# Kernel optimization log

Measured on AMD Instinct MI355X. Metric: run time of the kernel, lower is better.

Reference implementation:

```python
import jax, jax.numpy as jnp
import numpy as np

B, S, D, H = 2, 4096, 512, 8
HD = D // H  # 64


def setup_inputs() -> dict:
    key = jax.random.key(0)
    ks = jax.random.split(key, 9)
    def lin_init(kw, kb, fan_in, fan_out):
        bound = 1.0 / np.sqrt(fan_in)
        W = jax.random.uniform(kw, (fan_in, fan_out), minval=-bound, maxval=bound, dtype=jnp.float32)
        b = jax.random.uniform(kb, (fan_out,), minval=-bound, maxval=bound, dtype=jnp.float32)
        return W, b
    Wq, bq = lin_init(ks[0], ks[1], D, D)
    Wk, bk = lin_init(ks[2], ks[3], D, D)
    Wv, bv = lin_init(ks[4], ks[5], D, D)
    query = jax.random.normal(ks[6], (B, S, D), dtype=jnp.float32)
    key_in = jax.random.normal(ks[7], (B, S, D), dtype=jnp.float32)
    value = jax.random.normal(ks[8], (B, S, D), dtype=jnp.float32)
    return {"query": query, "key": key_in, "value": value,
            "Wq": Wq, "bq": bq, "Wk": Wk, "bk": bk, "Wv": Wv, "bv": bv}


def _split_heads(x):
    # [B, S, D] -> [B, H, S, HD]
    b, s, _ = x.shape
    return x.reshape(b, s, H, HD).transpose(0, 2, 1, 3)


def reference(query, key, value, Wq, bq, Wk, bk, Wv, bv):
    Q = _split_heads(query @ Wq + bq)
    K = _split_heads(key @ Wk + bk)
    V = _split_heads(value @ Wv + bv)
    scale = 1.0 / np.sqrt(HD).astype(np.float32)
    # scores: [B, H, Sq, Sk]
    scores = jnp.einsum('bhqd,bhkd->bhqk', Q, K) * scale
    weights = jax.nn.softmax(scores, axis=-1)
    att = jnp.einsum('bhqk,bhkd->bhqd', weights, V)
    # [B, H, S, HD] -> [B, S, D]
    return att.transpose(0, 2, 1, 3).reshape(query.shape[0], query.shape[1], D)
```

## Files before the change

kernel.cpp:

```cpp
#include <hip/hip_runtime.h>
#include <hip/hip_bf16.h>
#include <cstdint>


typedef __bf16   bf16x8 __attribute__((ext_vector_type(8)));
typedef _Float16 f16x8  __attribute__((ext_vector_type(8)));
typedef float    f32x4  __attribute__((ext_vector_type(4)));
typedef float    f32x16 __attribute__((ext_vector_type(16)));
typedef unsigned int   u32;
typedef unsigned int   u32x4 __attribute__((ext_vector_type(4)));
typedef unsigned short u16;

#define NB  2
#define SEQ 4096
#define DIM 512
#define NH  8
#define HD  64
#define WSZ (DIM * DIM)
#define QSZ (NB * NH * SEQ * HD)

__device__ __forceinline__ u16 f2bf(float f) {
    __bf16 h = (__bf16)f; return __builtin_bit_cast(u16, h);
}
__device__ __forceinline__ u16 f2h(float f) {
    _Float16 h = (_Float16)f; return __builtin_bit_cast(u16, h);
}
__device__ __forceinline__ u32 pack_pkrtz(float a, float b) {
    auto pk = __builtin_amdgcn_cvt_pkrtz(a, b);
    return __builtin_bit_cast(u32, pk);
}
__device__ __forceinline__ bf16x8 cvt8p(float4 a, float4 b) {
    bf16x8 o;
    o[0]=(__bf16)a.x; o[1]=(__bf16)a.y; o[2]=(__bf16)a.z; o[3]=(__bf16)a.w;
    o[4]=(__bf16)b.x; o[5]=(__bf16)b.y; o[6]=(__bf16)b.z; o[7]=(__bf16)b.w;
    return o;
}
__device__ __forceinline__ void dma16(const u16* g, u16* l) {
    __builtin_amdgcn_global_load_lds(
        (const __attribute__((address_space(1))) u32*)g,
        (__attribute__((address_space(3))) u32*)l, 16, 0, 0);
}

__global__ __launch_bounds__(256) void wt_kernel(
    const float* __restrict__ Wq, const float* __restrict__ Wk,
    const float* __restrict__ Wv, u16* __restrict__ wt)
{
    __shared__ u16 lT[64 * 65];
    const int p = blockIdx.z;
    const float* W = (p == 0) ? Wq : ((p == 1) ? Wk : Wv);
    u16* dst = wt + (size_t)p * WSZ;
    const int r0 = blockIdx.x * 64, c0 = blockIdx.y * 64;
    const int t = threadIdx.x;
#pragma unroll
    for (int i = 0; i < 16; i++) {
        int idx = i * 256 + t, row = idx >> 6, col = idx & 63;
        lT[col * 65 + row] = f2bf(W[(size_t)(r0 + row) * DIM + c0 + col]);
    }
    __syncthreads();
#pragma unroll
    for (int i = 0; i < 16; i++) {
        int idx = i * 256 + t, n = idx >> 6, k = idx & 63;
        dst[(size_t)(c0 + n) * DIM + r0 + k] = lT[n * 65 + k];
    }
}

__global__ __launch_bounds__(256) void proj_kernel(
    const float* __restrict__ xq, const float* __restrict__ xk,
    const float* __restrict__ xv, const u16* __restrict__ wt,
    const float* __restrict__ bq, const float* __restrict__ bk,
    const float* __restrict__ bv,
    u16* __restrict__ qb, u16* __restrict__ kbImg, u16* __restrict__ vtImg)
{
    __shared__ u16 smem[2 * 128 * 72];
    u16* lA = smem;
    u16* lB = smem + 128 * 72;

    const int tid = threadIdx.x;
    const int wave = tid >> 6, lane = tid & 63;
    const int l16 = lane & 15, quad = lane >> 4;
    const int wq = wave >> 1, wn = wave & 1;

    int p, mb, nb;
    {
        const int id = blockIdx.x;
        if (id < 512) { p = id >> 8; const int r = id & 255; mb = r >> 2; nb = r & 3; }
        else          { p = 2; const int r = id - 512; mb = r >> 6; nb = r & 63; }
    }
    const float* Xp = (p == 0) ? xq : ((p == 1) ? xk : xv);
    const u16*   Wp = wt + (size_t)p * WSZ;
    const bool cvtA = (p < 2);
    const float* Ff = cvtA ? (Xp + (size_t)mb * 128 * DIM) : (Xp + (size_t)nb * 128 * DIM);
    const u16*   Fb = cvtA ? (Wp + (size_t)nb * 128 * DIM) : (Wp + (size_t)mb * 128 * DIM);

    const float* pf[4]; const u16* pb[4]; int loff[4];
#pragma unroll
    for (int i = 0; i < 4; i++) {
        const int c = i * 256 + tid, row = c >> 3, seg = c & 7;
        pf[i] = Ff + (size_t)row * DIM + seg * 8;
        pb[i] = Fb + (size_t)row * DIM + seg * 8;
        loff[i] = row * 72 + seg * 8;
    }

    f32x4 acc[4][4];
#pragma unroll
    for (int ms = 0; ms < 4; ms++)
#pragma unroll
        for (int ns = 0; ns < 4; ns++)
#pragma unroll
            for (int j = 0; j < 4; j++) acc[ms][ns][j] = 0.f;

    float4 rf[8]; u32x4 rb[4];
#pragma unroll
    for (int i = 0; i < 4; i++) {
        rf[2*i]   = *(const float4*)(pf[i]);
        rf[2*i+1] = *(const float4*)(pf[i] + 4);
        rb[i]     = *(const u32x4*)(pb[i]);
        pf[i] += 64; pb[i] += 64;
    }

    for (int kt = 0; kt < 8; kt++) {
        __syncthreads();
#pragma unroll
        for (int i = 0; i < 4; i++) {
            if (cvtA) {
                *(bf16x8*)&lA[loff[i]] = cvt8p(rf[2*i], rf[2*i+1]);
                *(u32x4*)&lB[loff[i]]  = rb[i];
            } else {
                *(u32x4*)&lA[loff[i]]  = rb[i];
                *(bf16x8*)&lB[loff[i]] = cvt8p(rf[2*i], rf[2*i+1]);
            }
        }
        __syncthreads();
        if (kt < 7) {
#pragma unroll
            for (int i = 0; i < 4; i++) {
                rf[2*i]   = *(const float4*)(pf[i]);
                rf[2*i+1] = *(const float4*)(pf[i] + 4);
                rb[i]     = *(const u32x4*)(pb[i]);
                pf[i] += 64; pb[i] += 64;
            }
        }

        bf16x8 af[4][2];
#pragma unroll
        for (int ms = 0; ms < 4; ms++) {
            af[ms][0] = *(const bf16x8*)&lA[(wq * 64 + ms * 16 + l16) * 72 + quad * 8];
            af[ms][1] = *(const bf16x8*)&lA[(wq * 64 + ms * 16 + l16) * 72 + 32 + quad * 8];
        }
#pragma unroll
        for (int ns = 0; ns < 4; ns++) {
            bf16x8 b0 = *(const bf16x8*)&lB[(wn * 64 + ns * 16 + l16) * 72 + quad * 8];
            bf16x8 b1 = *(const bf16x8*)&lB[(wn * 64 + ns * 16 + l16) * 72 + 32 + quad * 8];
#pragma unroll
            for (int ms = 0; ms < 4; ms++) {
                acc[ms][ns] = __builtin_amdgcn_mfma_f32_16x16x32_bf16(af[ms][0], b0, acc[ms][ns], 0, 0, 0);
                acc[ms][ns] = __builtin_amdgcn_mfma_f32_16x16x32_bf16(af[ms][1], b1, acc[ms][ns], 0, 0, 0);
            }
        }
    }

    __syncthreads();
    if (p < 2) {
        const float* bias = p ? bk : bq;
        const float cs = (p == 0) ? 0.18033688011112042f : 1.0f;
        const int stl = wn * 2 + wq;
        const int hh = nb * 2 + wn;
#pragma unroll
        for (int ns = 0; ns < 4; ns++) {
            const int ch = ns * 16 + l16;
            const float bval = bias[hh * 64 + ch];
#pragma unroll
            for (int ms = 0; ms < 4; ms++)
#pragma unroll
                for (int rr = 0; rr < 4; rr++) {
                    const int sqL = ms * 16 + quad * 4 + rr;
                    const float v = (acc[ms][ns][rr] + bval) * cs;
                    int off;
                    if (p == 0) off = sqL * 64 + ch;
                    else        off = sqL * 64 +
                                      (((ch >> 3) ^ ((sqL ^ (sqL >> 3)) & 7)) << 3) + (ch & 7);
                    smem[stl * 4096 + off] = f2bf(v);
                }
        }
    } else {
        const int stl = wq * 2 + wn;
#pragma unroll
        for (int ms = 0; ms < 4; ms++)
#pragma unroll
            for (int rr = 0; rr < 4; rr++) {
                const int hd = ms * 16 + quad * 4 + rr;
                const float bval = bv[mb * 128 + wq * 64 + hd];
                const int swh = (hd ^ (hd >> 3)) & 7;
#pragma unroll
                for (int ns = 0; ns < 4; ns++) {
                    const int nl = ns * 16 + l16;
                    const int sqpL = (nl & ~12) | ((nl & 8) >> 1) | ((nl & 4) << 1);
                    smem[stl * 4096 + hd * 64 +
                         (((sqpL >> 3) ^ swh) << 3) + (sqpL & 7)] =
                        f2h(acc[ms][ns][rr] + bval);
                }
            }
    }
    __syncthreads();

    {
        u16* dstp; size_t gbase;
        if (p < 2) {
            const int hh = nb * 2 + (wave >> 1);
            const int b2 = mb >> 5;
            const int row0 = (mb * 128 + (wave & 1) * 64) & 4095;
            if (p == 0) { dstp = qb;    gbase = ((size_t)(b2 * NH + hh) * 4096 + row0) * 64; }
            else        { dstp = kbImg; gbase = ((size_t)((b2 * NH + hh) * 64 + (row0 >> 6))) * 4096; }
        } else {
            const int hh = mb * 2 + (wave >> 1);
            const int b2 = nb >> 5;
            const int nblk = (nb & 31) * 2 + (wave & 1);
            dstp = vtImg; gbase = ((size_t)((b2 * NH + hh) * 64 + nblk)) * 4096;
        }
#pragma unroll
        for (int e = 0; e < 8; e++) {
            const u32x4 vv = *(const u32x4*)&smem[wave * 4096 + e * 512 + lane * 8];
            *(u32x4*)(dstp + gbase + e * 512 + lane * 8) = vv;
        }
    }
}

__global__ __launch_bounds__(512, 4) void attn_kernel(
    const u16* __restrict__ qb, const u16* __restrict__ kbImg,
    const u16* __restrict__ vtImg, float* __restrict__ out)
{
    __shared__ u16 smem[2 * 4 * 4096];
    float* cmb = (float*)smem;

    const int tid = threadIdx.x;
    const int wave = tid >> 6, lane = tid & 63;
    const int m31 = lane & 31, h = lane >> 5;
    const int wq = wave >> 1, kh = wave & 1;

    const int blk = blockIdx.x;
    const int xcd = blk & 7, idx = blk >> 3;
    const int bh = xcd * 2 + (idx >> 5);
    const int qt = idx & 31;
    const int qbase = qt * 128 + wq * 32;

    bf16x8 qF[4];
#pragma unroll
    for (int c = 0; c < 4; c++)
        qF[c] = *(const bf16x8*)(qb + ((size_t)bh * SEQ + qbase + m31) * HD + c * 16 + h * 8);

    f32x16 O0, O1;
#pragma unroll
    for (int j = 0; j < 16; j++) { O0[j] = 0.f; O1[j] = 0.f; }
    float l_acc = 0.f;

    const int st  = wave >> 1;
    const int hw  = wave & 1;
    const u16* img = (st & 1) ? vtImg : kbImg;
    const u16* gp = img + ((size_t)(bh * 64 + (st >> 1) * 32)) * 4096 + hw * 2048 + lane * 8;
    {
        u16* lb = smem + st * 4096 + hw * 2048 + lane * 8;
#pragma unroll
        for (int e = 0; e < 4; e++) dma16(gp + e * 512, lb + e * 512);
        gp += 4096;
    }

    const int NT = 32;
    for (int it = 0; it < NT; it++) {
        __syncthreads();
        if (it + 1 < NT) {
            u16* lb = smem + ((((it + 1) & 1) * 4 + st)) * 4096 + hw * 2048 + lane * 8;
#pragma unroll
            for (int e = 0; e < 4; e++) dma16(gp + e * 512, lb + e * 512);
            gp += 4096;
        }
        const u16* sK = smem + (size_t)(((it & 1) * 4) + kh * 2) * 4096;
        const u16* sV = sK + 4096;

#pragma unroll
        for (int kg = 0; kg < 2; kg++) {
            const int rK = kg * 32 + m31;
            const int swK = (rK ^ (rK >> 3)) & 7;
            bf16x8 kA[4];
#pragma unroll
            for (int c = 0; c < 4; c++)
                kA[c] = *(const bf16x8*)&sK[(rK << 6) + (((2 * c + h) ^ swK) << 3)];

            const int swV0 = (m31 ^ (m31 >> 3)) & 7;
            const int rV1 = 32 + m31;
            const int swV1 = (rV1 ^ (rV1 >> 3)) & 7;
            f16x8 vA0[2], vA1[2];
#pragma unroll
            for (int c2 = 0; c2 < 2; c2++) {
                vA0[c2] = *(const f16x8*)&sV[(m31 << 6) + (((4 * kg + 2 * c2 + h) ^ swV0) << 3)];
                vA1[c2] = *(const f16x8*)&sV[(rV1 << 6) + (((4 * kg + 2 * c2 + h) ^ swV1) << 3)];
            }

            f32x16 Sv;
#pragma unroll
            for (int j = 0; j < 16; j++) Sv[j] = 0.f;
#pragma unroll
            for (int c = 0; c < 4; c++)
                Sv = __builtin_amdgcn_mfma_f32_32x32x16_bf16(kA[c], qF[c], Sv, 0, 0, 0);

            float ps = 0.f;
            u32 P32[8];
#pragma unroll
            for (int mm = 0; mm < 8; mm++) {
                const float e0 = __builtin_amdgcn_exp2f(Sv[2 * mm]);
                const float e1 = __builtin_amdgcn_exp2f(Sv[2 * mm + 1]);
                ps += e0 + e1;
                P32[mm] = pack_pkrtz(e0, e1);
            }
            l_acc += ps;

            u32x4 f0, f1;
            f0[0] = P32[0]; f0[1] = P32[1]; f0[2] = P32[2]; f0[3] = P32[3];
            f1[0] = P32[4]; f1[1] = P32[5]; f1[2] = P32[6]; f1[3] = P32[7];
            const f16x8 pf0 = __builtin_bit_cast(f16x8, f0);
            const f16x8 pf1 = __builtin_bit_cast(f16x8, f1);
            O0 = __builtin_amdgcn_mfma_f32_32x32x16_f16(vA0[0], pf0, O0, 0, 0, 0);
            O0 = __builtin_amdgcn_mfma_f32_32x32x16_f16(vA0[1], pf1, O0, 0, 0, 0);
            O1 = __builtin_amdgcn_mfma_f32_32x32x16_f16(vA1[0], pf0, O1, 0, 0, 0);
            O1 = __builtin_amdgcn_mfma_f32_32x32x16_f16(vA1[1], pf1, O1, 0, 0, 0);
        }
    }

    l_acc += __shfl_xor(l_acc, 32);
    __syncthreads();
    if (kh == 1) {
#pragma unroll
        for (int hg = 0; hg < 2; hg++)
#pragma unroll
            for (int mm = 0; mm < 4; mm++) {
                f32x4 o;
#pragma unroll
                for (int j = 0; j < 4; j++) o[j] = (hg ? O1 : O0)[4 * mm + j];
                *(f32x4*)&cmb[(((wq * 2 + hg) * 4 + mm) << 8) + lane * 4] = o;
            }
        cmb[8192 + wq * 64 + lane] = l_acc;
    }
    __syncthreads();

    if (kh == 0) {
        const int b = bh >> 3, hcol = bh & 7;
        const float lt = l_acc + cmb[8192 + wq * 64 + lane];
        const float inv = 1.0f / lt;
        const int sq = qbase + m31;
#pragma unroll
        for (int hg = 0; hg < 2; hg++)
#pragma unroll
            for (int mm = 0; mm < 4; mm++) {
                const f32x4 po = *(const f32x4*)&cmb[(((wq * 2 + hg) * 4 + mm) << 8) + lane * 4];
                f32x4 o;
#pragma unroll
                for (int j = 0; j < 4; j++)
                    o[j] = ((hg ? O1 : O0)[4 * mm + j] + po[j]) * inv;
                *(f32x4*)&out[(((size_t)(b * SEQ + sq)) << 9) + hcol * 64
                              + hg * 32 + 8 * mm + 4 * h] = o;
            }
    }
}

extern "C" void kernel_launch(void* const* d_in, const int* in_sizes, int n_in,
                              void* d_out, int out_size, void* d_ws, size_t ws_size,
                              hipStream_t stream)
{
    const float* q  = (const float*)d_in[0];
    const float* k  = (const float*)d_in[1];
    const float* v  = (const float*)d_in[2];
    const float* Wq = (const float*)d_in[3];
    const float* bq = (const float*)d_in[4];
    const float* Wk = (const float*)d_in[5];
    const float* bk = (const float*)d_in[6];
    const float* Wv = (const float*)d_in[7];
    const float* bv = (const float*)d_in[8];
    float* out = (float*)d_out;

    u16* wt  = (u16*)d_ws;
    u16* qbp = wt  + (size_t)3 * WSZ;
    u16* kbp = qbp + (size_t)QSZ;
    u16* vtp = kbp + (size_t)QSZ;

    wt_kernel  <<<dim3(8, 8, 3), 256, 0, stream>>>(Wq, Wk, Wv, wt);
    proj_kernel<<<dim3(768),     256, 0, stream>>>(q, k, v, wt, bq, bk, bv,
                                                   qbp, kbp, vtp);
    attn_kernel<<<dim3(512),     512, 0, stream>>>(qbp, kbp, vtp, out);
}
```

Baseline: 219.2 us.

## Pre-convert activations to bf16 tiled images and DMA-pipeline projection GEMM loads

```diff
diff --git a/kernel.cpp b/kernel.cpp
--- a/kernel.cpp
+++ b/kernel.cpp
@@ -17,6 +17,7 @@
 #define NH  8
 #define HD  64
 #define WSZ (DIM * DIM)
+#define XSZ (NB * SEQ * DIM)
 #define QSZ (NB * NH * SEQ * HD)
 
 __device__ __forceinline__ u16 f2bf(float f) {
@@ -41,65 +42,81 @@
         (__attribute__((address_space(3))) u32*)l, 16, 0, 0);
 }
 
+__global__ __launch_bounds__(256) void xcvt_kernel(
+    const float* __restrict__ xq, const float* __restrict__ xk,
+    const float* __restrict__ xv, u16* __restrict__ xb)
+{
+    const int id = blockIdx.x;
+    const int p = id >> 10, rest = id & 1023;
+    const int mtile = rest >> 4, kk = rest & 15;
+    const float* X = (p == 0) ? xq : ((p == 1) ? xk : xv);
+    const int t = threadIdx.x;
+    const int row = t >> 1, half = t & 1;
+    const float* src = X + ((size_t)(mtile * 128 + row)) * DIM + kk * 32 + half * 16;
+    u16* dst = xb + (size_t)p * XSZ + ((size_t)(mtile * 16 + kk)) * 4096 + row * 32;
+    const int sr = (row ^ (row >> 2)) & 3;
+    float4 a0 = ((const float4*)src)[0], a1 = ((const float4*)src)[1];
+    float4 a2 = ((const float4*)src)[2], a3 = ((const float4*)src)[3];
+    const int c0 = (half * 2) ^ sr, c1 = (half * 2 + 1) ^ sr;
+    *(bf16x8*)(dst + (c0 << 3)) = cvt8p(a0, a1);
+    *(bf16x8*)(dst + (c1 << 3)) = cvt8p(a2, a3);
+}
+
 __global__ __launch_bounds__(256) void wt_kernel(
     const float* __restrict__ Wq, const float* __restrict__ Wk,
-    const float* __restrict__ Wv, u16* __restrict__ wt)
+    const float* __restrict__ Wv, u16* __restrict__ wtImg)
 {
     __shared__ u16 lT[64 * 65];
     const int p = blockIdx.z;
     const float* W = (p == 0) ? Wq : ((p == 1) ? Wk : Wv);
-    u16* dst = wt + (size_t)p * WSZ;
     const int r0 = blockIdx.x * 64, c0 = blockIdx.y * 64;
     const int t = threadIdx.x;
 #pragma unroll
     for (int i = 0; i < 16; i++) {
-        int idx = i * 256 + t, row = idx >> 6, col = idx & 63;
-        lT[col * 65 + row] = f2bf(W[(size_t)(r0 + row) * DIM + c0 + col]);
-    }
-    __syncthreads();
-#pragma unroll
-    for (int i = 0; i < 16; i++) {
-        int idx = i * 256 + t, n = idx >> 6, k = idx & 63;
-        dst[(size_t)(c0 + n) * DIM + r0 + k] = lT[n * 65 + k];
+        int idx = i * 256 + t, rowk = idx >> 6, coln = idx & 63;
+        lT[coln * 65 + rowk] = f2bf(W[(size_t)(r0 + rowk) * DIM + c0 + coln]);
+    }
+    __syncthreads();
+#pragma unroll
+    for (int i = 0; i < 2; i++) {
+        const int idx = i * 256 + t;
+        const int nl = idx >> 3, ch = idx & 7;
+        const int n = c0 + nl;
+        const int row = n & 127, ntile = n >> 7;
+        const int kk = (r0 >> 5) + (ch >> 2);
+        const int sw = (ch & 3) ^ ((row ^ (row >> 2)) & 3);
+        u16* d = wtImg + (size_t)p * WSZ + ((size_t)(ntile * 16 + kk)) * 4096
+               + row * 32 + (sw << 3);
+#pragma unroll
+        for (int e = 0; e < 8; e++) d[e] = lT[nl * 65 + ch * 8 + e];
     }
 }
 
 __global__ __launch_bounds__(256) void proj_kernel(
-    const float* __restrict__ xq, const float* __restrict__ xk,
-    const float* __restrict__ xv, const u16* __restrict__ wt,
+    const u16* __restrict__ xb, const u16* __restrict__ wtImg,
     const float* __restrict__ bq, const float* __restrict__ bk,
     const float* __restrict__ bv,
     u16* __restrict__ qb, u16* __restrict__ kbImg, u16* __restrict__ vtImg)
 {
-    __shared__ u16 smem[2 * 128 * 72];
-    u16* lA = smem;
-    u16* lB = smem + 128 * 72;
+    __shared__ u16 smem[16384];
 
     const int tid = threadIdx.x;
     const int wave = tid >> 6, lane = tid & 63;
     const int l16 = lane & 15, quad = lane >> 4;
     const int wq = wave >> 1, wn = wave & 1;
 
-    int p, mb, nb;
-    {
-        const int id = blockIdx.x;
-        if (id < 512) { p = id >> 8; const int r = id & 255; mb = r >> 2; nb = r & 3; }
-        else          { p = 2; const int r = id - 512; mb = r >> 6; nb = r & 63; }
-    }
-    const float* Xp = (p == 0) ? xq : ((p == 1) ? xk : xv);
-    const u16*   Wp = wt + (size_t)p * WSZ;
-    const bool cvtA = (p < 2);
-    const float* Ff = cvtA ? (Xp + (size_t)mb * 128 * DIM) : (Xp + (size_t)nb * 128 * DIM);
-    const u16*   Fb = cvtA ? (Wp + (size_t)nb * 128 * DIM) : (Wp + (size_t)mb * 128 * DIM);
-
-    const float* pf[4]; const u16* pb[4]; int loff[4];
-#pragma unroll
-    for (int i = 0; i < 4; i++) {
-        const int c = i * 256 + tid, row = c >> 3, seg = c & 7;
-        pf[i] = Ff + (size_t)row * DIM + seg * 8;
-        pb[i] = Fb + (size_t)row * DIM + seg * 8;
-        loff[i] = row * 72 + seg * 8;
-    }
+    const int id = blockIdx.x;
+    const int xcd = id & 7, j = id >> 3;
+    const int p = j >> 5, t5 = j & 31;
+    int mb, nb;
+    if (p < 2) { mb = xcd * 8 + (t5 >> 2); nb = t5 & 3; }
+    else       { nb = xcd * 8 + (t5 >> 2); mb = t5 & 3; }
+
+    const u16* Abase = (p < 2) ? xb + (size_t)p * XSZ + (size_t)mb * 16 * 4096
+                               : wtImg + (size_t)2 * WSZ + (size_t)mb * 16 * 4096;
+    const u16* Bbase = (p < 2) ? wtImg + (size_t)p * WSZ + (size_t)nb * 16 * 4096
+                               : xb + (size_t)2 * XSZ + (size_t)nb * 16 * 4096;
+    const int doff = tid * 8;
 
     f32x4 acc[4][4];
 #pragma unroll
@@ -107,55 +124,44 @@
 #pragma unroll
         for (int ns = 0; ns < 4; ns++)
 #pragma unroll
-            for (int j = 0; j < 4; j++) acc[ms][ns][j] = 0.f;
-
-    float4 rf[8]; u32x4 rb[4];
-#pragma unroll
-    for (int i = 0; i < 4; i++) {
-        rf[2*i]   = *(const float4*)(pf[i]);
-        rf[2*i+1] = *(const float4*)(pf[i] + 4);
-        rb[i]     = *(const u32x4*)(pb[i]);
-        pf[i] += 64; pb[i] += 64;
-    }
-
-    for (int kt = 0; kt < 8; kt++) {
+            for (int jj = 0; jj < 4; jj++) acc[ms][ns][jj] = 0.f;
+
+#pragma unroll
+    for (int e = 0; e < 2; e++) {
+        dma16(Abase + e * 2048 + doff, smem + e * 2048 + doff);
+        dma16(Bbase + e * 2048 + doff, smem + 4096 + e * 2048 + doff);
+    }
+    Abase += 4096; Bbase += 4096;
+
+    for (int kt = 0; kt < 16; kt++) {
         __syncthreads();
-#pragma unroll
-        for (int i = 0; i < 4; i++) {
-            if (cvtA) {
-                *(bf16x8*)&lA[loff[i]] = cvt8p(rf[2*i], rf[2*i+1]);
-                *(u32x4*)&lB[loff[i]]  = rb[i];
-            } else {
-                *(u32x4*)&lA[loff[i]]  = rb[i];
-                *(bf16x8*)&lB[loff[i]] = cvt8p(rf[2*i], rf[2*i+1]);
-            }
-        }
-        __syncthreads();
-        if (kt < 7) {
-#pragma unroll
-            for (int i = 0; i < 4; i++) {
-                rf[2*i]   = *(const float4*)(pf[i]);
-                rf[2*i+1] = *(const float4*)(pf[i] + 4);
-                rb[i]     = *(const u32x4*)(pb[i]);
-                pf[i] += 64; pb[i] += 64;
-            }
-        }
-
-        bf16x8 af[4][2];
+        if (kt < 15) {
+            u16* lb = smem + ((kt + 1) & 1) * 8192;
+#pragma unroll
+            for (int e = 0; e < 2; e++) {
+                dma16(Abase + e * 2048 + doff, lb + e * 2048 + doff);
+                dma16(Bbase + e * 2048 + doff, lb + 4096 + e * 2048 + doff);
+            }
+            Abase += 4096; Bbase += 4096;
+        }
+        const u16* lA = smem + (kt & 1) * 8192;
+        const u16* lB = lA + 4096;
+
+        bf16x8 af[4];
 #pragma unroll
         for (int ms = 0; ms < 4; ms++) {
-            af[ms][0] = *(const bf16x8*)&lA[(wq * 64 + ms * 16 + l16) * 72 + quad * 8];
-            af[ms][1] = *(const bf16x8*)&lA[(wq * 64 + ms * 16 + l16) * 72 + 32 + quad * 8];
+            const int row = wq * 64 + ms * 16 + l16;
+            const int sr = (row ^ (row >> 2)) & 3;
+            af[ms] = *(const bf16x8*)&lA[row * 32 + ((quad ^ sr) << 3)];
         }
 #pragma unroll
         for (int ns = 0; ns < 4; ns++) {
-            bf16x8 b0 = *(const bf16x8*)&lB[(wn * 64 + ns * 16 + l16) * 72 + quad * 8];
-            bf16x8 b1 = *(const bf16x8*)&lB[(wn * 64 + ns * 16 + l16) * 72 + 32 + quad * 8];
-#pragma unroll
-            for (int ms = 0; ms < 4; ms++) {
-                acc[ms][ns] = __builtin_amdgcn_mfma_f32_16x16x32_bf16(af[ms][0], b0, acc[ms][ns], 0, 0, 0);
-                acc[ms][ns] = __builtin_amdgcn_mfma_f32_16x16x32_bf16(af[ms][1], b1, acc[ms][ns], 0, 0, 0);
-            }
+            const int rowb = wn * 64 + ns * 16 + l16;
+            const int sb = (rowb ^ (rowb >> 2)) & 3;
+            const bf16x8 b = *(const bf16x8*)&lB[rowb * 32 + ((quad ^ sb) << 3)];
+#pragma unroll
+            for (int ms = 0; ms < 4; ms++)
+                acc[ms][ns] = __builtin_amdgcn_mfma_f32_16x16x32_bf16(af[ms], b, acc[ms][ns], 0, 0, 0);
         }
     }
 
@@ -376,13 +382,15 @@
     const float* bv = (const float*)d_in[8];
     float* out = (float*)d_out;
 
-    u16* wt  = (u16*)d_ws;
-    u16* qbp = wt  + (size_t)3 * WSZ;
+    u16* xb  = (u16*)d_ws;
+    u16* wti = xb  + (size_t)3 * XSZ;
+    u16* qbp = wti + (size_t)3 * WSZ;
     u16* kbp = qbp + (size_t)QSZ;
     u16* vtp = kbp + (size_t)QSZ;
 
-    wt_kernel  <<<dim3(8, 8, 3), 256, 0, stream>>>(Wq, Wk, Wv, wt);
-    proj_kernel<<<dim3(768),     256, 0, stream>>>(q, k, v, wt, bq, bk, bv,
-                                                   qbp, kbp, vtp);
-    attn_kernel<<<dim3(512),     512, 0, stream>>>(qbp, kbp, vtp, out);
-}
+    xcvt_kernel<<<dim3(3072),   256, 0, stream>>>(q, k, v, xb);
+    wt_kernel  <<<dim3(8, 8, 3), 256, 0, stream>>>(Wq, Wk, Wv, wti);
+    proj_kernel<<<dim3(768),    256, 0, stream>>>(xb, wti, bq, bk, bv,
+                                                  qbp, kbp, vtp);
+    attn_kernel<<<dim3(512),    512, 0, stream>>>(qbp, kbp, vtp, out);
+}
```

Result: no change. 216.4 us (-1.3%).
